# Kernel tuning notes

Hardware: AMD Instinct MI355X
Metric: run time of the kernel (lower is better)

Reference implementation:

```python
import jax, jax.numpy as jnp
import numpy as np

D_MODEL = 1024
NUM_HEADS = 16
HEAD_DIM = D_MODEL // NUM_HEADS
HIDDEN = 4096
EPS = 1e-5


def setup_inputs() -> dict:
    key = jax.random.key(0)
    ks = jax.random.split(key, 10)
    s = 0.02
    return {
        "x": jax.random.normal(ks[0], (2, 2048, D_MODEL), dtype=jnp.float32),
        # attention projection weights stored as (in, out): y = x @ W
        "wq": jax.random.normal(ks[1], (D_MODEL, D_MODEL), dtype=jnp.float32) * s,
        "wk": jax.random.normal(ks[2], (D_MODEL, D_MODEL), dtype=jnp.float32) * s,
        "wv": jax.random.normal(ks[3], (D_MODEL, D_MODEL), dtype=jnp.float32) * s,
        "wo": jax.random.normal(ks[4], (D_MODEL, D_MODEL), dtype=jnp.float32) * s,
        # FFN
        "w1": jax.random.normal(ks[5], (D_MODEL, HIDDEN), dtype=jnp.float32) * s,
        "b1": jnp.zeros((HIDDEN,), dtype=jnp.float32),
        "w2": jax.random.normal(ks[6], (HIDDEN, D_MODEL), dtype=jnp.float32) * s,
        "b2": jnp.zeros((D_MODEL,), dtype=jnp.float32),
        # LayerNorms
        "g1": jnp.ones((D_MODEL,), dtype=jnp.float32),
        "be1": jnp.zeros((D_MODEL,), dtype=jnp.float32),
        "g2": jnp.ones((D_MODEL,), dtype=jnp.float32),
        "be2": jnp.zeros((D_MODEL,), dtype=jnp.float32),
    }


def _layernorm(x, g, b):
    mu = jnp.mean(x, axis=-1, keepdims=True)
    var = jnp.mean(jnp.square(x - mu), axis=-1, keepdims=True)
    return (x - mu) * jax.lax.rsqrt(var + EPS) * g + b


def _attention(x, wq, wk, wv, wo):
    B, S, D = x.shape
    q = (x @ wq).reshape(B, S, NUM_HEADS, HEAD_DIM)
    k = (x @ wk).reshape(B, S, NUM_HEADS, HEAD_DIM)
    v = (x @ wv).reshape(B, S, NUM_HEADS, HEAD_DIM)
    scores = jnp.einsum("bqhd,bkhd->bhqk", q, k) / jnp.sqrt(
        jnp.float32(HEAD_DIM)
    )
    causal = jnp.tril(jnp.ones((S, S), dtype=bool))
    scores = jnp.where(causal, scores, -jnp.inf)
    probs = jax.nn.softmax(scores, axis=-1)
    out = jnp.einsum("bhqk,bkhd->bqhd", probs, v).reshape(B, S, D)
    return out @ wo


def _ffn(x, w1, b1, w2, b2):
    return jax.nn.relu(x @ w1 + b1) @ w2 + b2


def reference(x, wq, wk, wv, wo, w1, b1, w2, b2, g1, be1, g2, be2):
    x = x + _attention(_layernorm(x, g1, be1), wq, wk, wv, wo)
    x = x + _ffn(_layernorm(x, g2, be2), w1, b1, w2, b2)
    return x
```

## Files before the change

### kernel.cpp

```cpp
#include <hip/hip_runtime.h>
#include <stdint.h>

typedef unsigned short bf16u;
typedef __attribute__((ext_vector_type(8))) __bf16 bf16x8;
typedef __attribute__((ext_vector_type(4))) float f32x4;
typedef __attribute__((ext_vector_type(4))) unsigned short u16x4;
typedef __attribute__((ext_vector_type(8))) unsigned short u16x8;

typedef __attribute__((address_space(1))) void gvoid_t;
typedef __attribute__((address_space(3))) void lvoid_t;

#define SEQ 2048
#define DM 1024
#define MN22 4194304
#define SCL 0.18033688f

__device__ __forceinline__ bf16u f2bf(float f) {
  union { float f; uint32_t u; } v; v.f = f;
  uint32_t u = v.u + 0x7fffu + ((v.u >> 16) & 1u);
  return (bf16u)(u >> 16);
}

__device__ __forceinline__ bf16u f2bf_hw(float f) {
  union { __bf16 h; bf16u u; } v; v.h = (__bf16)f; return v.u;
}

__device__ __forceinline__ float bf2f(bf16u b) {
  union { uint32_t u; float f; } v; v.u = (uint32_t)b << 16; return v.f;
}

__device__ __forceinline__ void async_copy16(const bf16u* g, const bf16u* l) {
  __builtin_amdgcn_global_load_lds((gvoid_t*)(uintptr_t)g,
                                   (lvoid_t*)(uint32_t)(uintptr_t)l,
                                   16, 0, 0);
}

#define VM_WAIT(n) asm volatile("s_waitcnt vmcnt(" #n ")" ::: "memory")
#define LGKM0()    asm volatile("s_waitcnt lgkmcnt(0)" ::: "memory")
#define BARRIER()  asm volatile("s_barrier" ::: "memory")

__global__ __launch_bounds__(256) void ln_kernel(const float* __restrict__ x,
                                                 const float* __restrict__ g,
                                                 const float* __restrict__ be,
                                                 bf16u* __restrict__ out) {
  const int row = blockIdx.x;
  const int t = threadIdx.x;
  const float4 v = ((const float4*)(x + (size_t)row * DM))[t];
  float s  = v.x + v.y + v.z + v.w;
  float ss = v.x * v.x + v.y * v.y + v.z * v.z + v.w * v.w;
#pragma unroll
  for (int m = 1; m < 64; m <<= 1) {
    s  += __shfl_xor(s, m, 64);
    ss += __shfl_xor(ss, m, 64);
  }
  __shared__ float red[2][4];
  const int wv = t >> 6, ln = t & 63;
  if (ln == 0) { red[0][wv] = s; red[1][wv] = ss; }
  __syncthreads();
  s  = red[0][0] + red[0][1] + red[0][2] + red[0][3];
  ss = red[1][0] + red[1][1] + red[1][2] + red[1][3];
  const float mu = s * (1.0f / DM);
  const float var = ss * (1.0f / DM) - mu * mu;
  const float rstd = rsqrtf(var + 1e-5f);
  const float4 gg = ((const float4*)g)[t];
  const float4 bb = ((const float4*)be)[t];
  u16x4 o;
  o[0] = f2bf((v.x - mu) * rstd * gg.x + bb.x);
  o[1] = f2bf((v.y - mu) * rstd * gg.y + bb.y);
  o[2] = f2bf((v.z - mu) * rstd * gg.z + bb.z);
  o[3] = f2bf((v.w - mu) * rstd * gg.w + bb.w);
  *(u16x4*)(out + (size_t)row * DM + t * 4) = o;
}

__global__ __launch_bounds__(256) void wtrans(const float* __restrict__ in,
                                              bf16u* __restrict__ out, int R, int C) {
  __shared__ float tile[32][33];
  const int c0 = blockIdx.x * 32, r0 = blockIdx.y * 32;
  const int tx = threadIdx.x, ty = threadIdx.y;
#pragma unroll
  for (int i = 0; i < 4; ++i)
    tile[ty + i * 8][tx] = in[(size_t)(r0 + ty + i * 8) * C + c0 + tx];
  __syncthreads();
#pragma unroll
  for (int i = 0; i < 4; ++i)
    out[(size_t)(c0 + ty + i * 8) * R + r0 + tx] = f2bf(tile[tx][ty + i * 8]);
}

__global__ __launch_bounds__(256) void wtrans4(const float* __restrict__ a,
                                               const float* __restrict__ b,
                                               const float* __restrict__ c,
                                               const float* __restrict__ d,
                                               bf16u* __restrict__ out) {
  const float* srcs[4] = {a, b, c, d};
  const float* in = srcs[blockIdx.z];
  bf16u* o = out + (size_t)blockIdx.z * 1024 * 1024;
  __shared__ float tile[32][33];
  const int c0 = blockIdx.x * 32, r0 = blockIdx.y * 32;
  const int tx = threadIdx.x, ty = threadIdx.y;
#pragma unroll
  for (int i = 0; i < 4; ++i)
    tile[ty + i * 8][tx] = in[(size_t)(r0 + ty + i * 8) * 1024 + c0 + tx];
  __syncthreads();
#pragma unroll
  for (int i = 0; i < 4; ++i)
    o[(size_t)(c0 + ty + i * 8) * 1024 + r0 + tx] = f2bf(tile[tx][ty + i * 8]);
}

__global__ __launch_bounds__(256) void reduce3(const bf16u* __restrict__ p01,
                                               const bf16u* __restrict__ p2,
                                               const float* __restrict__ bias,
                                               float* __restrict__ out) {
  const size_t i8 = ((size_t)blockIdx.x * 256 + threadIdx.x) * 8;
  const int col0 = (int)(i8 & 1023);
  const u16x8 a = *(const u16x8*)(p01 + i8);
  const u16x8 b = *(const u16x8*)(p01 + MN22 + i8);
  const u16x8 c = *(const u16x8*)(p2 + i8);
  const float4 o0 = *(const float4*)(out + i8);
  const float4 o1 = *(const float4*)(out + i8 + 4);
  const float4 b0 = *(const float4*)(bias + col0);
  const float4 b1 = *(const float4*)(bias + col0 + 4);
  float r[8];
#pragma unroll
  for (int j = 0; j < 8; ++j) r[j] = bf2f(a[j]) + bf2f(b[j]) + bf2f(c[j]);
  float4 w0, w1;
  w0.x = o0.x + r[0] + b0.x; w0.y = o0.y + r[1] + b0.y;
  w0.z = o0.z + r[2] + b0.z; w0.w = o0.w + r[3] + b0.w;
  w1.x = o1.x + r[4] + b1.x; w1.y = o1.y + r[5] + b1.y;
  w1.z = o1.z + r[6] + b1.z; w1.w = o1.w + r[7] + b1.w;
  *(float4*)(out + i8) = w0;
  *(float4*)(out + i8 + 4) = w1;
}

__global__ __launch_bounds__(512, 1) void gemm256(
    const bf16u* __restrict__ A, const bf16u* __restrict__ Bt,
    int M, int N, int K,
    const float* __restrict__ bias, bf16u* __restrict__ outB,
    bf16u* __restrict__ vt, int mode) {
  __shared__ bf16u sh[2][32768];
  const int t = threadIdx.x;
  const int ln = t & 63;
  const int wv = t >> 6;
  const int col16 = ln & 15, quad = ln >> 4;
  const int wm = wv >> 2, wn = wv & 3;

  const int nsplit = (mode == 6) ? 3 : 1;
  const int nbx = N >> 8;
  const int nwg = nbx * (M >> 8) * nsplit;
  const int cpx = nwg >> 3;
  const int bid = blockIdx.x;
  const int swz = (bid & 7) * cpx + (bid >> 3);
  const int tile = swz / nsplit, split = swz - tile * nsplit;
  const int m0 = (tile / nbx) << 8, n0 = (tile % nbx) << 8;
  const int tsteps = K >> 6;
  const int kbeg = (split * tsteps) / nsplit;
  const int nt = ((split + 1) * tsteps) / nsplit - kbeg;
  const size_t koff = (size_t)kbeg << 6;

  const bf16u* gsrc[4][2];
  int doff[4][2];
#pragma unroll
  for (int j = 0; j < 2; ++j) {
    const int c = t + (j << 9);
    const int lr = c >> 3, slot = (c & 7) ^ (lr & 7);
    const int ra = (lr & 63) + ((lr >> 6) << 7);
    const int rb = (lr & 31) + ((lr >> 5) << 6);
    gsrc[0][j] = A  + (size_t)(m0 + ra) * K + koff + slot * 8;
    gsrc[3][j] = A  + (size_t)(m0 + ra + 64) * K + koff + slot * 8;
    gsrc[1][j] = Bt + (size_t)(n0 + rb) * K + koff + slot * 8;
    gsrc[2][j] = Bt + (size_t)(n0 + rb + 32) * K + koff + slot * 8;
    doff[0][j] = c * 8;
    doff[3][j] = 8192 + c * 8;
    doff[1][j] = 16384 + c * 8;
    doff[2][j] = 24576 + c * 8;
  }

  const int sx = col16 & 7;
  int aoffs[4][2], boffs[2][2];
#pragma unroll
  for (int i = 0; i < 4; ++i)
#pragma unroll
    for (int kc = 0; kc < 2; ++kc)
      aoffs[i][kc] = (wm * 64 + i * 16 + col16) * 64 + (((kc << 2) + quad) ^ sx) * 8;
#pragma unroll
  for (int i = 0; i < 2; ++i)
#pragma unroll
    for (int kc = 0; kc < 2; ++kc)
      boffs[i][kc] = 16384 + (wn * 32 + i * 16 + col16) * 64 + (((kc << 2) + quad) ^ sx) * 8;

  f32x4 acc[8][4] = {};
  bf16x8 Af[4][2], Bf[4][2];

  auto stage = [&](int s, int b) {
#pragma unroll
    for (int j = 0; j < 2; ++j) {
      async_copy16(gsrc[s][j], &sh[b][doff[s][j]]);
      gsrc[s][j] += 64;
    }
  };
  auto readA = [&](int b, int mh) {
#pragma unroll
    for (int i = 0; i < 4; ++i)
#pragma unroll
      for (int kc = 0; kc < 2; ++kc)
        Af[i][kc] = *(const bf16x8*)(&sh[b][mh * 8192 + aoffs[i][kc]]);
  };
  auto readB = [&](int b, int nh) {
#pragma unroll
    for (int i = 0; i < 2; ++i)
#pragma unroll
      for (int kc = 0; kc < 2; ++kc)
        Bf[nh * 2 + i][kc] = *(const bf16x8*)(&sh[b][nh * 8192 + boffs[i][kc]]);
  };
  auto mfmaQ = [&](int mh, int nh) {
#pragma unroll
    for (int kc = 0; kc < 2; ++kc)
#pragma unroll
      for (int mi = 0; mi < 4; ++mi)
#pragma unroll
        for (int nl = 0; nl < 2; ++nl)
          acc[mh * 4 + mi][nh * 2 + nl] = __builtin_amdgcn_mfma_f32_16x16x32_bf16(
              Af[mi][kc], Bf[nh * 2 + nl][kc], acc[mh * 4 + mi][nh * 2 + nl], 0, 0, 0);
  };

  stage(0, 0); stage(1, 0); stage(2, 0); stage(3, 0);
  VM_WAIT(4);
  BARRIER();

  int bsel = 0;
  for (int kt = 0; kt < nt - 1; ++kt, bsel ^= 1) {
    const int bn = bsel ^ 1;
    readA(bsel, 0); readB(bsel, 0);
    stage(0, bn);
    BARRIER(); LGKM0();
    __builtin_amdgcn_s_setprio(1); mfmaQ(0, 0); __builtin_amdgcn_s_setprio(0);
    VM_WAIT(4); BARRIER();
    readB(bsel, 1);
    stage(1, bn);
    BARRIER(); LGKM0();
    __builtin_amdgcn_s_setprio(1); mfmaQ(0, 1); __builtin_amdgcn_s_setprio(0);
    VM_WAIT(4); BARRIER();
    readA(bsel, 1);
    stage(2, bn);
    BARRIER(); LGKM0();
    __builtin_amdgcn_s_setprio(1); mfmaQ(1, 0); __builtin_amdgcn_s_setprio(0);
    BARRIER();
    stage(3, bn);
    __builtin_amdgcn_s_setprio(1); mfmaQ(1, 1); __builtin_amdgcn_s_setprio(0);
    VM_WAIT(4); BARRIER();
  }
  readA(bsel, 0); readB(bsel, 0);
  BARRIER(); LGKM0();
  __builtin_amdgcn_s_setprio(1); mfmaQ(0, 0); __builtin_amdgcn_s_setprio(0);
  VM_WAIT(2); BARRIER();
  readB(bsel, 1);
  BARRIER(); LGKM0();
  __builtin_amdgcn_s_setprio(1); mfmaQ(0, 1); __builtin_amdgcn_s_setprio(0);
  VM_WAIT(0); BARRIER();
  readA(bsel, 1);
  LGKM0();
  __builtin_amdgcn_s_setprio(1); mfmaQ(1, 0); mfmaQ(1, 1); __builtin_amdgcn_s_setprio(0);

  if (mode == 6) {
    bf16u* pb = (split < 2) ? outB + (size_t)split * MN22 : vt;
#pragma unroll
    for (int mi = 0; mi < 8; ++mi) {
#pragma unroll
      for (int n = 0; n < 4; ++n) {
        const int col = n0 + wn * 64 + n * 16 + col16;
#pragma unroll
        for (int r = 0; r < 4; ++r) {
          const int row = m0 + wm * 128 + mi * 16 + quad * 4 + r;
          pb[(size_t)row * N + col] = f2bf(acc[mi][n][r]);
        }
      }
    }
    return;
  }
  if (mode == 5 && n0 >= 2048) {
#pragma unroll
    for (int mi = 0; mi < 8; ++mi) {
#pragma unroll
      for (int n = 0; n < 4; ++n) {
        const int col = n0 + wn * 64 + n * 16 + col16;
        const int hh = (col - 2048) >> 6, d = (col - 2048) & 63;
        const int row_base = m0 + wm * 128 + mi * 16 + quad * 4;
        const int bb = row_base >> 11, s = row_base & 2047;
        u16x4 o;
#pragma unroll
        for (int r = 0; r < 4; ++r) o[r] = f2bf(acc[mi][n][r]);
        *(u16x4*)(vt + (size_t)((bb * 16 + hh) * 64 + d) * SEQ + s) = o;
      }
    }
    return;
  }
  const float qscale = (mode == 5 && n0 < 1024) ? SCL : 1.0f;
  float bv[4];
  if (mode == 1) {
#pragma unroll
    for (int n = 0; n < 4; ++n) bv[n] = bias[n0 + wn * 64 + n * 16 + col16];
  }
#pragma unroll
  for (int mi = 0; mi < 8; ++mi) {
#pragma unroll
    for (int n = 0; n < 4; ++n) {
      const int col = n0 + wn * 64 + n * 16 + col16;
#pragma unroll
      for (int r = 0; r < 4; ++r) {
        const int row = m0 + wm * 128 + mi * 16 + quad * 4 + r;
        float v = acc[mi][n][r];
        if (mode == 1) v = fmaxf(v + bv[n], 0.0f);
        outB[(size_t)row * N + col] = f2bf(v * qscale);
      }
    }
  }
}

__global__ __launch_bounds__(256, 3) void gemm_bt64(
    const bf16u* __restrict__ A, const bf16u* __restrict__ Bt,
    int M, int N, int K,
    const float* __restrict__ bias, const float* __restrict__ resid,
    bf16u* __restrict__ outB, float* __restrict__ outF, int mode) {
  __shared__ bf16u As0[64 * 64], As1[64 * 64];
  __shared__ bf16u Bs0[128 * 64], Bs1[128 * 64];
  const int t = threadIdx.x;
  const int ln = t & 63;
  const int wv = t >> 6;
  const int col16 = ln & 15, quad = ln >> 4;

  const int nbx = gridDim.x;
  const int nwg = nbx * gridDim.y;
  const int cpx = nwg >> 3;
  const int flat = blockIdx.y * nbx + blockIdx.x;
  const int swz = (flat & 7) * cpx + (flat >> 3);
  const int m0 = (swz / nbx) * 64, n0 = (swz % nbx) * 128;

  const bf16u* gA[2];
  const bf16u* gB[4];
#pragma unroll
  for (int j = 0; j < 2; ++j) {
    const int c = t + 256 * j, row = c >> 3, slot = (c & 7) ^ (row & 7);
    gA[j] = A + (size_t)(m0 + row) * K + slot * 8;
  }
#pragma unroll
  for (int j = 0; j < 4; ++j) {
    const int c = t + 256 * j, row = c >> 3, slot = (c & 7) ^ (row & 7);
    gB[j] = Bt + (size_t)(n0 + row) * K + slot * 8;
  }

  f32x4 acc[4][2] = {};

  auto stage = [&](bf16u* dA, bf16u* dB) {
#pragma unroll
    for (int j = 0; j < 2; ++j) {
      async_copy16(gA[j], dA + (size_t)(t + 256 * j) * 8);
      gA[j] += 64;
    }
#pragma unroll
    for (int j = 0; j < 4; ++j) {
      async_copy16(gB[j], dB + (size_t)(t + 256 * j) * 8);
      gB[j] += 64;
    }
  };
  auto compute = [&](const bf16u* sA, const bf16u* sB) {
    bf16x8 af[4][2], bfv[2][2];
#pragma unroll
    for (int mi = 0; mi < 4; ++mi) {
      const int row = mi * 16 + col16;
#pragma unroll
      for (int kc = 0; kc < 2; ++kc)
        af[mi][kc] = *(const bf16x8*)(sA + row * 64 + (((kc << 2) + quad) ^ (row & 7)) * 8);
    }
#pragma unroll
    for (int ni = 0; ni < 2; ++ni) {
      const int row = wv * 32 + ni * 16 + col16;
#pragma unroll
      for (int kc = 0; kc < 2; ++kc)
        bfv[ni][kc] = *(const bf16x8*)(sB + row * 64 + (((kc << 2) + quad) ^ (row & 7)) * 8);
    }
#pragma unroll
    for (int kc = 0; kc < 2; ++kc)
#pragma unroll
      for (int mi = 0; mi < 4; ++mi)
#pragma unroll
        for (int ni = 0; ni < 2; ++ni)
          acc[mi][ni] = __builtin_amdgcn_mfma_f32_16x16x32_bf16(af[mi][kc], bfv[ni][kc],
                                                                acc[mi][ni], 0, 0, 0);
  };

  const int niter = K >> 6;
  stage(As0, Bs0);
  for (int k = 0; k < niter; k += 2) {
    stage(As1, Bs1);
    VM_WAIT(6);
    BARRIER();
    compute(As0, Bs0);
    BARRIER();
    if (k + 2 < niter) {
      stage(As0, Bs0);
      VM_WAIT(6);
    } else {
      VM_WAIT(0);
    }
    BARRIER();
    compute(As1, Bs1);
    BARRIER();
  }

#pragma unroll
  for (int mi = 0; mi < 4; ++mi) {
#pragma unroll
    for (int ni = 0; ni < 2; ++ni) {
      const int col = n0 + wv * 32 + ni * 16 + col16;
#pragma unroll
      for (int r = 0; r < 4; ++r) {
        const int row = m0 + mi * 16 + quad * 4 + r;
        float v = acc[mi][ni][r];
        if (mode == 1 || mode == 3) v += bias[col];
        if (mode == 1) v = fmaxf(v, 0.0f);
        if (mode >= 2) {
          outF[(size_t)row * N + col] = v + resid[(size_t)row * N + col];
        } else {
          outB[(size_t)row * N + col] = f2bf(v);
        }
      }
    }
  }
}

#define PST 132
__global__ __launch_bounds__(256, 3) void attn_kernel(const bf16u* __restrict__ qkv,
                                                      const bf16u* __restrict__ vt,
                                                      bf16u* __restrict__ out) {
  __shared__ bf16u Ks[128 * 64];
  __shared__ bf16u Vts[2 * 64 * 64];
  __shared__ bf16u pbuf[4][16 * PST];
  __shared__ float lred[4][16];
  const int t = threadIdx.x;
  const int wv = t >> 6, ln = t & 63;
  const int col = ln & 15, quad = ln >> 4;
  const int bh = blockIdx.x, b = bh >> 4, h = bh & 15;
  const int strip = 31 - blockIdx.y;
  const int q0 = strip * 64;
  const int qw = q0 + wv * 16;
  const int qmax = qw + 15;
  const int ntiles = (q0 >> 7) + 1;

  int krow[4], kslot[4], vrow[4], vsub[4], vslot[4];
  const bf16u *kl[4], *vl[4];
#pragma unroll
  for (int j = 0; j < 4; ++j) {
    const int c = t + 256 * j;
    krow[j] = c >> 3; kslot[j] = (c & 7) ^ (krow[j] & 7);
    const int rem = c & 511;
    vsub[j] = c >> 9; vrow[j] = rem >> 3; vslot[j] = (rem & 7) ^ (vrow[j] & 7);
    kl[j] = Ks + (size_t)c * 8;
    vl[j] = Vts + (size_t)c * 8;
  }

  auto stageK = [&](int kb) {
    const int kbase = kb * 128;
#pragma unroll
    for (int j = 0; j < 4; ++j)
      async_copy16(qkv + (size_t)(b * SEQ + kbase + krow[j]) * 3072 + 1024 + h * 64 + kslot[j] * 8, kl[j]);
  };
  auto stageV = [&](int kb) {
    const int kbase = kb * 128;
#pragma unroll
    for (int j = 0; j < 4; ++j)
      async_copy16(vt + (size_t)(bh * 64 + vrow[j]) * SEQ + kbase + vsub[j] * 64 + vslot[j] * 8, vl[j]);
  };

  bf16x8 qf0, qf1;
  {
    const size_t qoff = (size_t)(b * SEQ + qw + col) * 3072 + h * 64 + quad * 8;
    qf0 = *(const bf16x8*)(qkv + qoff);
    qf1 = *(const bf16x8*)(qkv + qoff + 32);
  }
  f32x4 po[4] = {};
  float ll[4] = {};

  stageK(0);
  stageV(0);
  VM_WAIT(4);
  BARRIER();

  for (int kb = 0; kb < ntiles; ++kb) {
    const int kbase = kb * 128;
    if (kb < ntiles - 1) {
      f32x4 sc[8];
#pragma unroll
      for (int n = 0; n < 8; ++n) {
        const int kr = n * 16 + col;
        const bf16x8 k0 = *(const bf16x8*)(Ks + kr * 64 + (quad ^ (kr & 7)) * 8);
        const bf16x8 k1 = *(const bf16x8*)(Ks + kr * 64 + ((4 + quad) ^ (kr & 7)) * 8);
        f32x4 z = {};
        z = __builtin_amdgcn_mfma_f32_16x16x32_bf16(qf0, k0, z, 0, 0, 0);
        sc[n] = __builtin_amdgcn_mfma_f32_16x16x32_bf16(qf1, k1, z, 0, 0, 0);
      }
#pragma unroll
      for (int r = 0; r < 4; ++r) {
#pragma unroll
        for (int n = 0; n < 8; ++n) {
          const float e = exp2f(sc[n][r]);
          ll[r] += e;
          pbuf[wv][(quad * 4 + r) * PST + n * 16 + col] = f2bf_hw(e);
        }
      }
    } else {
      f32x4 sc[8];
      bool act[8];
#pragma unroll
      for (int n = 0; n < 8; ++n) {
        act[n] = (kbase + n * 16) <= qmax;
        if (act[n]) {
          const int kr = n * 16 + col;
          const bf16x8 k0 = *(const bf16x8*)(Ks + kr * 64 + (quad ^ (kr & 7)) * 8);
          const bf16x8 k1 = *(const bf16x8*)(Ks + kr * 64 + ((4 + quad) ^ (kr & 7)) * 8);
          f32x4 z = {};
          z = __builtin_amdgcn_mfma_f32_16x16x32_bf16(qf0, k0, z, 0, 0, 0);
          sc[n] = __builtin_amdgcn_mfma_f32_16x16x32_bf16(qf1, k1, z, 0, 0, 0);
        }
      }
#pragma unroll
      for (int r = 0; r < 4; ++r) {
        const int q = qw + quad * 4 + r;
#pragma unroll
        for (int n = 0; n < 8; ++n) {
          float e = 0.0f;
          if (act[n]) {
            float v = sc[n][r];
            v = (kbase + n * 16 + col <= q) ? v : -1e30f;
            e = exp2f(v);
          }
          ll[r] += e;
          pbuf[wv][(quad * 4 + r) * PST + n * 16 + col] = f2bf_hw(e);
        }
      }
    }
    LGKM0();
    bf16x8 pa[4];
#pragma unroll
    for (int kc = 0; kc < 4; ++kc)
      pa[kc] = *(const bf16x8*)(&pbuf[wv][col * PST + kc * 32 + quad * 8]);
    VM_WAIT(0);
    BARRIER();
    if (kb + 1 < ntiles) stageK(kb + 1);
    if (kb < ntiles - 1) {
#pragma unroll
      for (int n = 0; n < 4; ++n) {
        const int vr = n * 16 + col;
#pragma unroll
        for (int kc = 0; kc < 4; ++kc) {
          const bf16x8 vfr = *(const bf16x8*)(Vts + (kc >> 1) * 4096 + vr * 64 +
                                              (((kc & 1) * 4 + quad) ^ (vr & 7)) * 8);
          po[n] = __builtin_amdgcn_mfma_f32_16x16x32_bf16(vfr, pa[kc], po[n], 0, 0, 0);
        }
      }
    } else {
#pragma unroll
      for (int n = 0; n < 4; ++n) {
        const int vr = n * 16 + col;
#pragma unroll
        for (int kc = 0; kc < 4; ++kc)
          if (kbase + kc * 32 <= qmax) {
            const bf16x8 vfr = *(const bf16x8*)(Vts + (kc >> 1) * 4096 + vr * 64 +
                                                (((kc & 1) * 4 + quad) ^ (vr & 7)) * 8);
            po[n] = __builtin_amdgcn_mfma_f32_16x16x32_bf16(vfr, pa[kc], po[n], 0, 0, 0);
          }
      }
    }
    if (kb + 1 < ntiles) {
      LGKM0();
      BARRIER();
      stageV(kb + 1);
      VM_WAIT(4);
      BARRIER();
    }
  }

#pragma unroll
  for (int m = 1; m < 16; m <<= 1)
#pragma unroll
    for (int r = 0; r < 4; ++r) ll[r] += __shfl_xor(ll[r], m, 64);
  if (col == 0) {
#pragma unroll
    for (int r = 0; r < 4; ++r) lred[wv][quad * 4 + r] = ll[r];
  }
  LGKM0();
  const float inv = 1.0f / lred[wv][col];
#pragma unroll
  for (int n = 0; n < 4; ++n) {
    u16x4 o;
#pragma unroll
    for (int r = 0; r < 4; ++r) o[r] = f2bf(po[n][r] * inv);
    *(u16x4*)(out + (size_t)(b * SEQ + qw + col) * DM + h * 64 + n * 16 + quad * 4) = o;
  }
}

extern "C" void kernel_launch(void* const* d_in, const int* in_sizes, int n_in,
                              void* d_out, int out_size, void* d_ws, size_t ws_size,
                              hipStream_t stream) {
  const float* x   = (const float*)d_in[0];
  const float* wq  = (const float*)d_in[1];
  const float* wk  = (const float*)d_in[2];
  const float* wvv = (const float*)d_in[3];
  const float* wo  = (const float*)d_in[4];
  const float* w1  = (const float*)d_in[5];
  const float* b1  = (const float*)d_in[6];
  const float* w2  = (const float*)d_in[7];
  const float* b2  = (const float*)d_in[8];
  const float* g1  = (const float*)d_in[9];
  const float* be1 = (const float*)d_in[10];
  const float* g2  = (const float*)d_in[11];
  const float* be2 = (const float*)d_in[12];
  float* out = (float*)d_out;

  char* ws = (char*)d_ws;
  bf16u* wqkv_t = (bf16u*)(ws);
  bf16u* wo_t   = (bf16u*)(ws +  6291456);
  bf16u* w1_t   = (bf16u*)(ws +  8388608);
  bf16u* w2_t   = (bf16u*)(ws + 16777216);
  bf16u* lnbuf  = (bf16u*)(ws + 25165824);
  bf16u* qkv    = (bf16u*)(ws + 33554432);
  bf16u* vtb    = (bf16u*)(ws + 58720256);
  bf16u* h1     = (bf16u*)(ws + 33554432);
  bf16u* attn   = lnbuf;
  bf16u* p01 = (bf16u*)(ws);
  bf16u* p2  = (bf16u*)(ws + 25165824);

  const dim3 tb32(32, 8);
  wtrans4<<<dim3(32, 32, 4), tb32, 0, stream>>>(wq, wk, wvv, wo, wqkv_t);
  wtrans<<<dim3(128, 32), tb32, 0, stream>>>(w1, w1_t, 1024, 4096);
  wtrans<<<dim3(32, 128), tb32, 0, stream>>>(w2, w2_t, 4096, 1024);

  ln_kernel<<<4096, 256, 0, stream>>>(x, g1, be1, lnbuf);
  gemm256<<<192, 512, 0, stream>>>(lnbuf, wqkv_t, 4096, 3072, 1024,
                                   nullptr, qkv, vtb, 5);
  attn_kernel<<<dim3(32, 32), 256, 0, stream>>>(qkv, vtb, attn);
  gemm_bt64<<<dim3(8, 64), 256, 0, stream>>>(attn, wo_t, 4096, 1024, 1024,
                                             nullptr, x, nullptr, out, 2);
  ln_kernel<<<4096, 256, 0, stream>>>(out, g2, be2, lnbuf);
  gemm256<<<256, 512, 0, stream>>>(lnbuf, w1_t, 4096, 4096, 1024,
                                   b1, h1, nullptr, 1);
  gemm256<<<192, 512, 0, stream>>>(h1, w2_t, 4096, 1024, 4096,
                                   nullptr, p01, p2, 6);
  reduce3<<<2048, 256, 0, stream>>>(p01, p2, b2, out);
}
```

Measured before the change: 322.3 us.

## Double attention query tile per block to 128 rows, reuse K/V staging

Each attention block now covers 128 query rows, with 32 rows per wave handled as two 16-row groups, instead of 64 rows. Each K and V fragment read from shared memory therefore feeds twice as many MFMAs, and the amount of K/V loaded from global memory per query row is halved. The grid becomes 512 one-dimensional blocks with a strip order that pairs long and short causal strips, and launch bounds drop to 2 blocks per CU. In exchange each thread holds more registers and the pbuf staging area doubles, which lowers occupancy. Causal masking in the final tile also becomes coarser.

Result: slower. 391.6 us (+21.5%).

```diff
diff --git a/kernel.cpp b/kernel.cpp
--- a/kernel.cpp
+++ b/kernel.cpp
@@ -428,22 +428,23 @@
 }
 
 #define PST 132
-__global__ __launch_bounds__(256, 3) void attn_kernel(const bf16u* __restrict__ qkv,
+__global__ __launch_bounds__(256, 2) void attn_kernel(const bf16u* __restrict__ qkv,
                                                       const bf16u* __restrict__ vt,
                                                       bf16u* __restrict__ out) {
   __shared__ bf16u Ks[128 * 64];
   __shared__ bf16u Vts[2 * 64 * 64];
-  __shared__ bf16u pbuf[4][16 * PST];
-  __shared__ float lred[4][16];
+  __shared__ bf16u pbuf[4][32 * PST];
+  __shared__ float lred[4][32];
   const int t = threadIdx.x;
   const int wv = t >> 6, ln = t & 63;
   const int col = ln & 15, quad = ln >> 4;
-  const int bh = blockIdx.x, b = bh >> 4, h = bh & 15;
-  const int strip = 31 - blockIdx.y;
-  const int q0 = strip * 64;
-  const int qw = q0 + wv * 16;
-  const int qmax = qw + 15;
-  const int ntiles = (q0 >> 7) + 1;
+  const int i = blockIdx.x;
+  const int bh = i & 31, b = bh >> 4, h = bh & 15;
+  const int k8 = (i & 255) >> 5;
+  const int strip = (i < 256) ? (15 - k8) : k8;
+  const int q0 = strip << 7;
+  const int qw = q0 + wv * 32;
+  const int ntiles = strip + 1;
 
   int krow[4], kslot[4], vrow[4], vsub[4], vslot[4];
   const bf16u *kl[4], *vl[4];
@@ -470,14 +471,15 @@
       async_copy16(vt + (size_t)(bh * 64 + vrow[j]) * SEQ + kbase + vsub[j] * 64 + vslot[j] * 8, vl[j]);
   };
 
-  bf16x8 qf0, qf1;
-  {
-    const size_t qoff = (size_t)(b * SEQ + qw + col) * 3072 + h * 64 + quad * 8;
-    qf0 = *(const bf16x8*)(qkv + qoff);
-    qf1 = *(const bf16x8*)(qkv + qoff + 32);
-  }
-  f32x4 po[4] = {};
-  float ll[4] = {};
+  bf16x8 qf[2][2];
+#pragma unroll
+  for (int g = 0; g < 2; ++g) {
+    const size_t qoff = (size_t)(b * SEQ + qw + g * 16 + col) * 3072 + h * 64 + quad * 8;
+    qf[g][0] = *(const bf16x8*)(qkv + qoff);
+    qf[g][1] = *(const bf16x8*)(qkv + qoff + 32);
+  }
+  f32x4 po[2][4] = {};
+  float ll[2][4] = {};
 
   stageK(0);
   stageV(0);
@@ -487,61 +489,75 @@
   for (int kb = 0; kb < ntiles; ++kb) {
     const int kbase = kb * 128;
     if (kb < ntiles - 1) {
-      f32x4 sc[8];
+      f32x4 sc[2][8];
 #pragma unroll
       for (int n = 0; n < 8; ++n) {
         const int kr = n * 16 + col;
         const bf16x8 k0 = *(const bf16x8*)(Ks + kr * 64 + (quad ^ (kr & 7)) * 8);
         const bf16x8 k1 = *(const bf16x8*)(Ks + kr * 64 + ((4 + quad) ^ (kr & 7)) * 8);
-        f32x4 z = {};
-        z = __builtin_amdgcn_mfma_f32_16x16x32_bf16(qf0, k0, z, 0, 0, 0);
-        sc[n] = __builtin_amdgcn_mfma_f32_16x16x32_bf16(qf1, k1, z, 0, 0, 0);
-      }
-#pragma unroll
-      for (int r = 0; r < 4; ++r) {
-#pragma unroll
-        for (int n = 0; n < 8; ++n) {
-          const float e = exp2f(sc[n][r]);
-          ll[r] += e;
-          pbuf[wv][(quad * 4 + r) * PST + n * 16 + col] = f2bf_hw(e);
-        }
-      }
+        f32x4 za = {}, zb = {};
+        za = __builtin_amdgcn_mfma_f32_16x16x32_bf16(qf[0][0], k0, za, 0, 0, 0);
+        sc[0][n] = __builtin_amdgcn_mfma_f32_16x16x32_bf16(qf[0][1], k1, za, 0, 0, 0);
+        zb = __builtin_amdgcn_mfma_f32_16x16x32_bf16(qf[1][0], k0, zb, 0, 0, 0);
+        sc[1][n] = __builtin_amdgcn_mfma_f32_16x16x32_bf16(qf[1][1], k1, zb, 0, 0, 0);
+      }
+#pragma unroll
+      for (int g = 0; g < 2; ++g)
+#pragma unroll
+        for (int r = 0; r < 4; ++r)
+#pragma unroll
+          for (int n = 0; n < 8; ++n) {
+            const float e = exp2f(sc[g][n][r]);
+            ll[g][r] += e;
+            pbuf[wv][(g * 16 + quad * 4 + r) * PST + n * 16 + col] = f2bf_hw(e);
+          }
     } else {
-      f32x4 sc[8];
-      bool act[8];
+      f32x4 sc[2][8];
+      bool acta[8], actb[8];
 #pragma unroll
       for (int n = 0; n < 8; ++n) {
-        act[n] = (kbase + n * 16) <= qmax;
-        if (act[n]) {
+        acta[n] = (kbase + n * 16) <= qw + 15;
+        actb[n] = (kbase + n * 16) <= qw + 31;
+        if (actb[n]) {
           const int kr = n * 16 + col;
           const bf16x8 k0 = *(const bf16x8*)(Ks + kr * 64 + (quad ^ (kr & 7)) * 8);
           const bf16x8 k1 = *(const bf16x8*)(Ks + kr * 64 + ((4 + quad) ^ (kr & 7)) * 8);
-          f32x4 z = {};
-          z = __builtin_amdgcn_mfma_f32_16x16x32_bf16(qf0, k0, z, 0, 0, 0);
-          sc[n] = __builtin_amdgcn_mfma_f32_16x16x32_bf16(qf1, k1, z, 0, 0, 0);
+          f32x4 zb = {};
+          zb = __builtin_amdgcn_mfma_f32_16x16x32_bf16(qf[1][0], k0, zb, 0, 0, 0);
+          sc[1][n] = __builtin_amdgcn_mfma_f32_16x16x32_bf16(qf[1][1], k1, zb, 0, 0, 0);
+          if (acta[n]) {
+            f32x4 za = {};
+            za = __builtin_amdgcn_mfma_f32_16x16x32_bf16(qf[0][0], k0, za, 0, 0, 0);
+            sc[0][n] = __builtin_amdgcn_mfma_f32_16x16x32_bf16(qf[0][1], k1, za, 0, 0, 0);
+          }
         }
       }
 #pragma unroll
-      for (int r = 0; r < 4; ++r) {
-        const int q = qw + quad * 4 + r;
-#pragma unroll
-        for (int n = 0; n < 8; ++n) {
-          float e = 0.0f;
-          if (act[n]) {
-            float v = sc[n][r];
-            v = (kbase + n * 16 + col <= q) ? v : -1e30f;
-            e = exp2f(v);
+      for (int g = 0; g < 2; ++g)
+#pragma unroll
+        for (int r = 0; r < 4; ++r) {
+          const int q = qw + g * 16 + quad * 4 + r;
+#pragma unroll
+          for (int n = 0; n < 8; ++n) {
+            float e = 0.0f;
+            const bool act = g ? actb[n] : acta[n];
+            if (act) {
+              float v = sc[g][n][r];
+              v = (kbase + n * 16 + col <= q) ? v : -1e30f;
+              e = exp2f(v);
+            }
+            ll[g][r] += e;
+            pbuf[wv][(g * 16 + quad * 4 + r) * PST + n * 16 + col] = f2bf_hw(e);
           }
-          ll[r] += e;
-          pbuf[wv][(quad * 4 + r) * PST + n * 16 + col] = f2bf_hw(e);
         }
-      }
     }
     LGKM0();
-    bf16x8 pa[4];
-#pragma unroll
-    for (int kc = 0; kc < 4; ++kc)
-      pa[kc] = *(const bf16x8*)(&pbuf[wv][col * PST + kc * 32 + quad * 8]);
+    bf16x8 pa[2][4];
+#pragma unroll
+    for (int g = 0; g < 2; ++g)
+#pragma unroll
+      for (int kc = 0; kc < 4; ++kc)
+        pa[g][kc] = *(const bf16x8*)(&pbuf[wv][(g * 16 + col) * PST + kc * 32 + quad * 8]);
     VM_WAIT(0);
     BARRIER();
     if (kb + 1 < ntiles) stageK(kb + 1);
@@ -553,7 +569,8 @@
         for (int kc = 0; kc < 4; ++kc) {
           const bf16x8 vfr = *(const bf16x8*)(Vts + (kc >> 1) * 4096 + vr * 64 +
                                               (((kc & 1) * 4 + quad) ^ (vr & 7)) * 8);
-          po[n] = __builtin_amdgcn_mfma_f32_16x16x32_bf16(vfr, pa[kc], po[n], 0, 0, 0);
+          po[0][n] = __builtin_amdgcn_mfma_f32_16x16x32_bf16(vfr, pa[0][kc], po[0][n], 0, 0, 0);
+          po[1][n] = __builtin_amdgcn_mfma_f32_16x16x32_bf16(vfr, pa[1][kc], po[1][n], 0, 0, 0);
         }
       }
     } else {
@@ -562,10 +579,12 @@
         const int vr = n * 16 + col;
 #pragma unroll
         for (int kc = 0; kc < 4; ++kc)
-          if (kbase + kc * 32 <= qmax) {
+          if (kbase + kc * 32 <= qw + 31) {
             const bf16x8 vfr = *(const bf16x8*)(Vts + (kc >> 1) * 4096 + vr * 64 +
                                                 (((kc & 1) * 4 + quad) ^ (vr & 7)) * 8);
-            po[n] = __builtin_amdgcn_mfma_f32_16x16x32_bf16(vfr, pa[kc], po[n], 0, 0, 0);
+            po[1][n] = __builtin_amdgcn_mfma_f32_16x16x32_bf16(vfr, pa[1][kc], po[1][n], 0, 0, 0);
+            if (kbase + kc * 32 <= qw + 15)
+              po[0][n] = __builtin_amdgcn_mfma_f32_16x16x32_bf16(vfr, pa[0][kc], po[0][n], 0, 0, 0);
           }
       }
     }
@@ -581,19 +600,26 @@
 #pragma unroll
   for (int m = 1; m < 16; m <<= 1)
 #pragma unroll
-    for (int r = 0; r < 4; ++r) ll[r] += __shfl_xor(ll[r], m, 64);
+    for (int g = 0; g < 2; ++g)
+#pragma unroll
+      for (int r = 0; r < 4; ++r) ll[g][r] += __shfl_xor(ll[g][r], m, 64);
   if (col == 0) {
 #pragma unroll
-    for (int r = 0; r < 4; ++r) lred[wv][quad * 4 + r] = ll[r];
+    for (int g = 0; g < 2; ++g)
+#pragma unroll
+      for (int r = 0; r < 4; ++r) lred[wv][g * 16 + quad * 4 + r] = ll[g][r];
   }
   LGKM0();
-  const float inv = 1.0f / lred[wv][col];
-#pragma unroll
-  for (int n = 0; n < 4; ++n) {
-    u16x4 o;
-#pragma unroll
-    for (int r = 0; r < 4; ++r) o[r] = f2bf(po[n][r] * inv);
-    *(u16x4*)(out + (size_t)(b * SEQ + qw + col) * DM + h * 64 + n * 16 + quad * 4) = o;
+#pragma unroll
+  for (int g = 0; g < 2; ++g) {
+    const float inv = 1.0f / lred[wv][g * 16 + col];
+#pragma unroll
+    for (int n = 0; n < 4; ++n) {
+      u16x4 o;
+#pragma unroll
+      for (int r = 0; r < 4; ++r) o[r] = f2bf(po[g][n][r] * inv);
+      *(u16x4*)(out + (size_t)(b * SEQ + qw + g * 16 + col) * DM + h * 64 + n * 16 + quad * 4) = o;
+    }
   }
 }
 
@@ -636,7 +662,7 @@
   ln_kernel<<<4096, 256, 0, stream>>>(x, g1, be1, lnbuf);
   gemm256<<<192, 512, 0, stream>>>(lnbuf, wqkv_t, 4096, 3072, 1024,
                                    nullptr, qkv, vtb, 5);
-  attn_kernel<<<dim3(32, 32), 256, 0, stream>>>(qkv, vtb, attn);
+  attn_kernel<<<512, 256, 0, stream>>>(qkv, vtb, attn);
   gemm_bt64<<<dim3(8, 64), 256, 0, stream>>>(attn, wo_t, 4096, 1024, 1024,
                                              nullptr, x, nullptr, out, 2);
   ln_kernel<<<4096, 256, 0, stream>>>(out, g2, be2, lnbuf);
```
